# Optimization experiments

Hardware: AMD Instinct MI355X
Metric: run time of the kernel (lower is better)

The kernel has to match this reference:

```python
import jax, jax.numpy as jnp
import numpy as np

NUM_EXPERTS = 8
TOP_K = 2


def setup_inputs() -> dict:
    key = jax.random.key(0)
    k0, k1, k2, k3, k4 = jax.random.split(key, 5)
    T, D, F, E = 4096, 2048, 4096, NUM_EXPERTS  # tokens, hidden, intermediate, experts
    s_in = 1.0 / np.sqrt(D).astype(np.float32)
    s_mid = 1.0 / np.sqrt(F).astype(np.float32)
    return {
        "hidden_states": jax.random.normal(k0, (T, D), jnp.float32),
        "gate_w": jax.random.normal(k1, (D, E), jnp.float32) * s_in,   # router gate (no bias)
        "w1": jax.random.normal(k2, (E, D, F), jnp.float32) * s_in,     # expert gate proj
        "w3": jax.random.normal(k3, (E, D, F), jnp.float32) * s_in,     # expert up proj
        "w2": jax.random.normal(k4, (E, F, D), jnp.float32) * s_mid,    # expert down proj
    }


def reference(hidden_states, gate_w, w1, w3, w2):
    x = hidden_states  # [T, D] (original flattens any leading dims)
    # Router: logits in fp32 (router_logits.float()), softmax over ALL experts,
    # take top-k WITHOUT renormalization (renormalize=False).
    logits = (x @ gate_w).astype(jnp.float32)            # [T, E]
    probs = jax.nn.softmax(logits, axis=-1)              # [T, E]
    topk_w, topk_i = jax.lax.top_k(probs, TOP_K)         # [T, K]
    # Dense combine weights: zero for non-selected experts. [T, E]
    combine = jnp.sum(
        jax.nn.one_hot(topk_i, NUM_EXPERTS, dtype=x.dtype) * topk_w[..., None],
        axis=1,
    )

    # SwiGLU experts, vmapped over the expert axis (fixed, small E).
    def expert_fn(w1e, w3e, w2e):
        return (jax.nn.silu(x @ w1e) * (x @ w3e)) @ w2e  # [T, D]

    expert_out = jax.vmap(expert_fn)(w1, w3, w2)         # [E, T, D]
    return jnp.einsum("te,etd->td", combine, expert_out)  # [T, D]
```

## Files before the change

### kernel.cpp

```cpp
#include <hip/hip_runtime.h>
#include <hip/hip_bf16.h>

#define TK 4096
#define DD 2048
#define FF 4096
#define NE 8
#define BM 128
#define BN 128
#define BKR 32
#define BKG 64

typedef __attribute__((ext_vector_type(8))) short bf16x8;
typedef __attribute__((ext_vector_type(4))) short bf16x4;
typedef __attribute__((ext_vector_type(4))) float f32x4;

__device__ __forceinline__ unsigned short f2bf(float f) {
  return __builtin_bit_cast(unsigned short, __float2bfloat16(f));
}

__device__ __forceinline__ void gl16(const unsigned short* g, unsigned short* l) {
  __builtin_amdgcn_global_load_lds(
      (const __attribute__((address_space(1))) unsigned int*)g,
      (__attribute__((address_space(3))) unsigned int*)l, 16, 0, 0);
}

__device__ __forceinline__ int g_swz(int row) { return ((row >> 1) & 3) ^ ((row >> 3) & 3); }
__device__ __forceinline__ int swzoff(int row, int bir) {
  return row * 64 + ((((bir >> 4) ^ g_swz(row)) & 3) << 4) + (bir & 15);
}
__device__ __forceinline__ int permB(int f) {
  return (f & 0x60) | ((f & 3) << 3) | ((f >> 2) & 7);
}

__global__ void k_router(const float* __restrict__ x, const float* __restrict__ gw,
                         int* __restrict__ cnt, int* __restrict__ ltok,
                         float* __restrict__ lw, unsigned short* __restrict__ xb) {
  int tok = (blockIdx.x * blockDim.x + threadIdx.x) >> 6;
  int lane = threadIdx.x & 63;
  if (tok >= TK) return;
  const float* xr = x + (size_t)tok * DD;
  float a0=0,a1=0,a2=0,a3=0,a4=0,a5=0,a6=0,a7=0;
  for (int p = 0; p < DD / 256; ++p) {
    int d0 = p * 256 + lane * 4;
    f32x4 xv = *(const f32x4*)(xr + d0);
    if (xb) {
      bf16x4 t;
      t[0] = (short)f2bf(xv[0]); t[1] = (short)f2bf(xv[1]);
      t[2] = (short)f2bf(xv[2]); t[3] = (short)f2bf(xv[3]);
      *(bf16x4*)(xb + (size_t)tok * DD + d0) = t;
    }
#pragma unroll
    for (int j = 0; j < 4; ++j) {
      float xs = xv[j];
      const f32x4* g = (const f32x4*)(gw + (size_t)(d0 + j) * NE);
      f32x4 g0 = g[0], g1 = g[1];
      a0 += xs * g0[0]; a1 += xs * g0[1]; a2 += xs * g0[2]; a3 += xs * g0[3];
      a4 += xs * g1[0]; a5 += xs * g1[1]; a6 += xs * g1[2]; a7 += xs * g1[3];
    }
  }
#pragma unroll
  for (int s = 32; s > 0; s >>= 1) {
    a0 += __shfl_xor(a0, s, 64); a1 += __shfl_xor(a1, s, 64);
    a2 += __shfl_xor(a2, s, 64); a3 += __shfl_xor(a3, s, 64);
    a4 += __shfl_xor(a4, s, 64); a5 += __shfl_xor(a5, s, 64);
    a6 += __shfl_xor(a6, s, 64); a7 += __shfl_xor(a7, s, 64);
  }
  if (lane == 0) {
    float p_[NE] = {a0, a1, a2, a3, a4, a5, a6, a7};
    float m = p_[0];
#pragma unroll
    for (int e = 1; e < NE; ++e) m = fmaxf(m, p_[e]);
    float ssum = 0.f;
#pragma unroll
    for (int e = 0; e < NE; ++e) { p_[e] = __expf(p_[e] - m); ssum += p_[e]; }
    float inv = 1.f / ssum;
    int i1 = 0; float b1 = p_[0];
#pragma unroll
    for (int e = 1; e < NE; ++e) if (p_[e] > b1) { b1 = p_[e]; i1 = e; }
    int i2 = -1; float b2 = -1.f;
#pragma unroll
    for (int e = 0; e < NE; ++e) if (e != i1 && p_[e] > b2) { b2 = p_[e]; i2 = e; }
    int s1 = atomicAdd(&cnt[i1], 1);
    ltok[i1 * TK + s1] = tok; lw[i1 * TK + s1] = b1 * inv;
    int s2 = atomicAdd(&cnt[i2], 1);
    ltok[i2 * TK + s2] = tok; lw[i2 * TK + s2] = b2 * inv;
  }
}

__global__ void k_prefix(const int* __restrict__ cnt, int* __restrict__ off) {
  if (threadIdx.x == 0) {
    int a = 0;
#pragma unroll
    for (int e = 0; e < NE; ++e) { off[e] = a; a += cnt[e]; }
    off[NE] = a;
  }
}

__global__ void k_tr(const float* __restrict__ src0, unsigned short* __restrict__ dst0,
                     int R, int C) {
  const int e = blockIdx.z;
  const float* src = src0 + (size_t)e * R * C;
  unsigned short* dst = dst0 + (size_t)e * R * C;
  const int r0 = blockIdx.y * 64, c0 = blockIdx.x * 64;
  const int tid = threadIdx.x;
  __shared__ unsigned short t[64][66];
#pragma unroll
  for (int p = 0; p < 4; ++p) {
    int r = p * 16 + (tid >> 4);
    int c = (tid & 15) * 4;
    f32x4 v = *(const f32x4*)(src + (size_t)(r0 + r) * C + c0 + c);
#pragma unroll
    for (int j = 0; j < 4; ++j) t[c + j][r] = f2bf(v[j]);
  }
  __syncthreads();
#pragma unroll
  for (int p = 0; p < 2; ++p) {
    int c = p * 32 + (tid >> 3);
    int r = (tid & 7) * 8;
    bf16x8 o;
#pragma unroll
    for (int j = 0; j < 8; ++j) o[j] = (short)t[c][r + j];
    *(bf16x8*)(dst + (size_t)(c0 + c) * R + r0 + r) = o;
  }
}


__global__ __launch_bounds__(256, 2)
void k_gemm1g(const unsigned short* __restrict__ xb, const unsigned short* __restrict__ w1t,
              const unsigned short* __restrict__ w3t, const int* __restrict__ cnt,
              const int* __restrict__ off, const int* __restrict__ ltok,
              const float* __restrict__ lw, unsigned short* __restrict__ H) {
  const int e = blockIdx.z;
  const int ce = cnt[e];
  const int m0 = blockIdx.y * BM;
  if (m0 >= ce) return;
  const int n0 = blockIdx.x * BN;
  const int tid = threadIdx.x, lane = tid & 63, w = tid >> 6;
  const int wr = w >> 1, wc = w & 1;
  const unsigned short* W1 = w1t + (size_t)e * FF * DD;
  const unsigned short* W3 = w3t + (size_t)e * FF * DD;
  const int base = off[e];

  __shared__ __align__(16) unsigned short As[BM * BKG];
  __shared__ __align__(16) unsigned short B1s[BN * BKG];
  __shared__ __align__(16) unsigned short B3s[BN * BKG];

  const int swz8 = ((lane & 7) ^ ((lane >> 3) & 7)) * 8;
  const unsigned short* aSrc[4];
  const unsigned short* b1Src[4];
  const unsigned short* b3Src[4];
#pragma unroll
  for (int i = 0; i < 4; ++i) {
    int row = w * 32 + i * 8 + (lane >> 3);
    int gm = m0 + row;
    int tok = (gm < ce) ? ltok[e * TK + gm] : 0;
    aSrc[i]  = xb + (size_t)tok * DD + swz8;
    b1Src[i] = W1 + (size_t)(n0 + row) * DD + swz8;
    b3Src[i] = W3 + (size_t)(n0 + row) * DD + swz8;
  }

  int aOff[4][2], bOff[4][2];
#pragma unroll
  for (int m = 0; m < 4; ++m) {
    int row = wr * 64 + m * 16 + (lane & 15);
#pragma unroll
    for (int kk = 0; kk < 2; ++kk) {
      int c = kk * 4 + (lane >> 4);
      aOff[m][kk] = row * 128 + ((c ^ (row & 7)) << 4);
    }
  }
#pragma unroll
  for (int n = 0; n < 4; ++n) {
    int row = wc * 64 + n * 16 + (lane & 15);
#pragma unroll
    for (int kk = 0; kk < 2; ++kk) {
      int c = kk * 4 + (lane >> 4);
      bOff[n][kk] = row * 128 + ((c ^ (row & 7)) << 4);
    }
  }

  f32x4 acc1[4][4], acc3[4][4];
#pragma unroll
  for (int m = 0; m < 4; ++m)
#pragma unroll
    for (int n = 0; n < 4; ++n)
#pragma unroll
      for (int j = 0; j < 4; ++j) { acc1[m][n][j] = 0.f; acc3[m][n][j] = 0.f; }

  const int NT = DD / BKG;
  for (int kt = 0; kt < NT; ++kt) {
#pragma unroll
    for (int i = 0; i < 4; ++i) {
      const int seg = w * 4 + i;
      gl16(aSrc[i],  &As[seg * 512]);
      gl16(b1Src[i], &B1s[seg * 512]);
      gl16(b3Src[i], &B3s[seg * 512]);
      aSrc[i] += BKG; b1Src[i] += BKG; b3Src[i] += BKG;
    }
    __syncthreads();
#pragma unroll
    for (int kk = 0; kk < 2; ++kk) {
      bf16x8 af[4];
#pragma unroll
      for (int m = 0; m < 4; ++m) af[m] = *(const bf16x8*)((const char*)As + aOff[m][kk]);
#pragma unroll
      for (int n = 0; n < 4; ++n) {
        bf16x8 b1 = *(const bf16x8*)((const char*)B1s + bOff[n][kk]);
        bf16x8 b3 = *(const bf16x8*)((const char*)B3s + bOff[n][kk]);
#pragma unroll
        for (int m = 0; m < 4; ++m) {
          acc1[m][n] = __builtin_amdgcn_mfma_f32_16x16x32_bf16(af[m], b1, acc1[m][n], 0, 0, 0);
          acc3[m][n] = __builtin_amdgcn_mfma_f32_16x16x32_bf16(af[m], b3, acc3[m][n], 0, 0, 0);
        }
      }
    }
    __syncthreads();
  }

#pragma unroll
  for (int m = 0; m < 4; ++m) {
    const int rbase = wr * 64 + m * 16 + ((lane >> 4) << 2);
    float wts[4]; bool val[4];
#pragma unroll
    for (int j = 0; j < 4; ++j) {
      int r = m0 + rbase + j;
      val[j] = r < ce;
      wts[j] = val[j] ? lw[e * TK + r] : 0.f;
    }
#pragma unroll
    for (int n = 0; n < 4; ++n) {
      const int col = n0 + wc * 64 + n * 16 + (lane & 15);
#pragma unroll
      for (int j = 0; j < 4; ++j) {
        if (!val[j]) continue;
        float s1 = acc1[m][n][j], s3 = acc3[m][n][j];
        float h = s1 / (1.f + __expf(-s1)) * s3 * wts[j];
        H[(size_t)(base + m0 + rbase + j) * FF + col] = f2bf(h);
      }
    }
  }
}

__global__ __launch_bounds__(256, 3)
void k_gemm2g(const unsigned short* __restrict__ H, const unsigned short* __restrict__ w2t,
              const int* __restrict__ cnt, const int* __restrict__ off,
              const int* __restrict__ ltok, float* __restrict__ out) {
  const int e = blockIdx.z;
  const int ce = cnt[e];
  const int m0 = blockIdx.y * BM;
  if (m0 >= ce) return;
  const int n0 = blockIdx.x * BN;
  const int tid = threadIdx.x, lane = tid & 63, w = tid >> 6;
  const int wr = w >> 1, wc = w & 1;
  const unsigned short* W2 = w2t + (size_t)e * DD * FF;
  const int base = off[e];

  __shared__ __align__(16) unsigned short As[BM * BKG];
  __shared__ __align__(16) unsigned short Bs[BN * BKG];

  const int swz8 = ((lane & 7) ^ ((lane >> 3) & 7)) * 8;
  const unsigned short* aSrc[4];
  const unsigned short* bSrc[4];
#pragma unroll
  for (int i = 0; i < 4; ++i) {
    int row = w * 32 + i * 8 + (lane >> 3);
    int gm = m0 + row;
    int hr = (gm < ce) ? gm : 0;
    aSrc[i] = H + (size_t)(base + hr) * FF + swz8;
    bSrc[i] = W2 + (size_t)(n0 + row) * FF + swz8;
  }

  int aOff[4][2], bOff[4][2];
#pragma unroll
  for (int m = 0; m < 4; ++m) {
    int row = wr * 64 + m * 16 + (lane & 15);
#pragma unroll
    for (int kk = 0; kk < 2; ++kk) {
      int c = kk * 4 + (lane >> 4);
      aOff[m][kk] = row * 128 + ((c ^ (row & 7)) << 4);
    }
  }
#pragma unroll
  for (int n = 0; n < 4; ++n) {
    int row = wc * 64 + n * 16 + (lane & 15);
#pragma unroll
    for (int kk = 0; kk < 2; ++kk) {
      int c = kk * 4 + (lane >> 4);
      bOff[n][kk] = row * 128 + ((c ^ (row & 7)) << 4);
    }
  }

  f32x4 acc[4][4];
#pragma unroll
  for (int m = 0; m < 4; ++m)
#pragma unroll
    for (int n = 0; n < 4; ++n)
#pragma unroll
      for (int j = 0; j < 4; ++j) acc[m][n][j] = 0.f;

  const int NT = FF / BKG;
  for (int kt = 0; kt < NT; ++kt) {
#pragma unroll
    for (int i = 0; i < 4; ++i) {
      const int seg = w * 4 + i;
      gl16(aSrc[i], &As[seg * 512]);
      gl16(bSrc[i], &Bs[seg * 512]);
      aSrc[i] += BKG; bSrc[i] += BKG;
    }
    __syncthreads();
#pragma unroll
    for (int kk = 0; kk < 2; ++kk) {
      bf16x8 af[4];
#pragma unroll
      for (int m = 0; m < 4; ++m) af[m] = *(const bf16x8*)((const char*)As + aOff[m][kk]);
#pragma unroll
      for (int n = 0; n < 4; ++n) {
        bf16x8 bf = *(const bf16x8*)((const char*)Bs + bOff[n][kk]);
#pragma unroll
        for (int m = 0; m < 4; ++m)
          acc[m][n] = __builtin_amdgcn_mfma_f32_16x16x32_bf16(af[m], bf, acc[m][n], 0, 0, 0);
      }
    }
    __syncthreads();
  }

#pragma unroll
  for (int m = 0; m < 4; ++m) {
    const int rbase = wr * 64 + m * 16 + ((lane >> 4) << 2);
    int toks[4]; bool val[4];
#pragma unroll
    for (int j = 0; j < 4; ++j) {
      int r = m0 + rbase + j;
      val[j] = r < ce;
      toks[j] = val[j] ? ltok[e * TK + r] : 0;
    }
#pragma unroll
    for (int n = 0; n < 4; ++n) {
      const int col = n0 + wc * 64 + n * 16 + (lane & 15);
#pragma unroll
      for (int j = 0; j < 4; ++j)
        if (val[j]) atomicAdd(out + (size_t)toks[j] * DD + col, acc[m][n][j]);
    }
  }
}

__global__ __launch_bounds__(256, 2)
void k_gemm1(const float* __restrict__ x, const float* __restrict__ w1g,
             const float* __restrict__ w3g, const int* __restrict__ cnt,
             const int* __restrict__ off, const int* __restrict__ ltok,
             const float* __restrict__ lw, unsigned short* __restrict__ H) {
  const int e = blockIdx.z;
  const int ce = cnt[e];
  const int m0 = blockIdx.y * BM;
  if (m0 >= ce) return;
  const int n0 = blockIdx.x * BN;
  const int tid = threadIdx.x, lane = tid & 63, wv = tid >> 6;
  const int wr = wv >> 1, wc = wv & 1;
  const float* W1 = w1g + (size_t)e * DD * FF;
  const float* W3 = w3g + (size_t)e * DD * FF;
  const int base = off[e];

  __shared__ unsigned short As[2][BM * BKR];
  __shared__ unsigned short B1s[2][BN * BKR];
  __shared__ unsigned short B3s[2][BN * BKR];

  const int arow = tid >> 1, ah = tid & 1;
  const float* xrow = (m0 + arow < ce) ? (x + (size_t)ltok[e * TK + (m0 + arow)] * DD) : nullptr;
  const int dblk = tid >> 5, fblk = tid & 31;

  const int kb = (lane >> 4) * 16;
  int aOff[4], bOff[4], wAoff[4], wBoff[4];
#pragma unroll
  for (int m = 0; m < 4; ++m) aOff[m] = swzoff(wr * 64 + m * 16 + (lane & 15), kb);
#pragma unroll
  for (int n = 0; n < 4; ++n) bOff[n] = swzoff(permB(wc * 64 + n * 16 + (lane & 15)), kb);
#pragma unroll
  for (int j = 0; j < 4; ++j) {
    wAoff[j] = swzoff(arow, ah * 32 + j * 8);
    wBoff[j] = swzoff(permB(fblk * 4 + j), dblk * 8);
  }

  f32x4 acc1[4][4], acc3[4][4];
#pragma unroll
  for (int m = 0; m < 4; ++m)
#pragma unroll
    for (int n = 0; n < 4; ++n)
#pragma unroll
      for (int j = 0; j < 4; ++j) { acc1[m][n][j] = 0.f; acc3[m][n][j] = 0.f; }

  f32x4 av[4], v1[4], v3[4];

  auto LOAD = [&](int kt) {
    const int k0 = kt * BKR;
#pragma unroll
    for (int j = 0; j < 4; ++j) {
      if (xrow) av[j] = *(const f32x4*)(xrow + k0 + ah * 16 + j * 4);
      else { av[j][0] = 0.f; av[j][1] = 0.f; av[j][2] = 0.f; av[j][3] = 0.f; }
    }
    const float* p1 = W1 + (size_t)(k0 + dblk * 4) * FF + (n0 + fblk * 4);
    const float* p3 = W3 + (size_t)(k0 + dblk * 4) * FF + (n0 + fblk * 4);
#pragma unroll
    for (int r = 0; r < 4; ++r) {
      v1[r] = *(const f32x4*)(p1 + (size_t)r * FF);
      v3[r] = *(const f32x4*)(p3 + (size_t)r * FF);
    }
  };
  auto STORE = [&](int buf) {
#pragma unroll
    for (int j = 0; j < 4; ++j) {
      bf16x4 t;
      t[0] = (short)f2bf(av[j][0]); t[1] = (short)f2bf(av[j][1]);
      t[2] = (short)f2bf(av[j][2]); t[3] = (short)f2bf(av[j][3]);
      *(bf16x4*)((char*)As[buf] + wAoff[j]) = t;
    }
#pragma unroll
    for (int j = 0; j < 4; ++j) {
      bf16x4 t1, t3;
      t1[0] = (short)f2bf(v1[0][j]); t1[1] = (short)f2bf(v1[1][j]);
      t1[2] = (short)f2bf(v1[2][j]); t1[3] = (short)f2bf(v1[3][j]);
      t3[0] = (short)f2bf(v3[0][j]); t3[1] = (short)f2bf(v3[1][j]);
      t3[2] = (short)f2bf(v3[2][j]); t3[3] = (short)f2bf(v3[3][j]);
      *(bf16x4*)((char*)B1s[buf] + wBoff[j]) = t1;
      *(bf16x4*)((char*)B3s[buf] + wBoff[j]) = t3;
    }
  };

  LOAD(0); STORE(0);
  int cur = 0;
  const int NT = DD / BKR;
  for (int kt = 0; kt < NT; ++kt) {
    if (kt + 1 < NT) LOAD(kt + 1);
    __syncthreads();
    bf16x8 af[4];
#pragma unroll
    for (int m = 0; m < 4; ++m) af[m] = *(const bf16x8*)((const char*)As[cur] + aOff[m]);
#pragma unroll
    for (int n = 0; n < 4; ++n) {
      bf16x8 b1 = *(const bf16x8*)((const char*)B1s[cur] + bOff[n]);
      bf16x8 b3 = *(const bf16x8*)((const char*)B3s[cur] + bOff[n]);
#pragma unroll
      for (int m = 0; m < 4; ++m) {
        acc1[m][n] = __builtin_amdgcn_mfma_f32_16x16x32_bf16(af[m], b1, acc1[m][n], 0, 0, 0);
        acc3[m][n] = __builtin_amdgcn_mfma_f32_16x16x32_bf16(af[m], b3, acc3[m][n], 0, 0, 0);
      }
    }
    if (kt + 1 < NT) STORE(cur ^ 1);
    cur ^= 1;
  }

#pragma unroll
  for (int m = 0; m < 4; ++m) {
    const int rbase = wr * 64 + m * 16 + ((lane >> 4) << 2);
    float wts[4]; bool val[4];
#pragma unroll
    for (int j = 0; j < 4; ++j) {
      int r = m0 + rbase + j;
      val[j] = r < ce;
      wts[j] = val[j] ? lw[e * TK + r] : 0.f;
    }
#pragma unroll
    for (int n = 0; n < 4; ++n) {
      const int col = n0 + wc * 64 + n * 16 + (lane & 15);
#pragma unroll
      for (int j = 0; j < 4; ++j) {
        if (!val[j]) continue;
        float s1 = acc1[m][n][j], s3 = acc3[m][n][j];
        float h = s1 / (1.f + __expf(-s1)) * s3 * wts[j];
        H[(size_t)(base + m0 + rbase + j) * FF + col] = f2bf(h);
      }
    }
  }
}

__global__ __launch_bounds__(256, 2)
void k_gemm2(const unsigned short* __restrict__ H, const float* __restrict__ w2g,
             const int* __restrict__ cnt, const int* __restrict__ off,
             const int* __restrict__ ltok, float* __restrict__ out) {
  const int e = blockIdx.z;
  const int ce = cnt[e];
  const int m0 = blockIdx.y * BM;
  if (m0 >= ce) return;
  const int n0 = blockIdx.x * BN;
  const int tid = threadIdx.x, lane = tid & 63, wv = tid >> 6;
  const int wr = wv >> 1, wc = wv & 1;
  const float* W2 = w2g + (size_t)e * FF * DD;
  const int base = off[e];

  __shared__ unsigned short As[2][BM * BKR];
  __shared__ unsigned short Bs[2][BN * BKR];

  const int arow = tid >> 1, ah = tid & 1;
  const bool aval = (m0 + arow) < ce;
  const unsigned short* hrow = H + (size_t)(base + m0 + arow) * FF;
  const int kblk = tid >> 5, nblk = tid & 31;

  const int kb = (lane >> 4) * 16;
  int aOff[4], bOff[4], wAoff[2], wBoff[4];
#pragma unroll
  for (int m = 0; m < 4; ++m) aOff[m] = swzoff(wr * 64 + m * 16 + (lane & 15), kb);
#pragma unroll
  for (int n = 0; n < 4; ++n) bOff[n] = swzoff(permB(wc * 64 + n * 16 + (lane & 15)), kb);
#pragma unroll
  for (int j = 0; j < 2; ++j) wAoff[j] = swzoff(arow, ah * 32 + j * 16);
#pragma unroll
  for (int j = 0; j < 4; ++j) wBoff[j] = swzoff(permB(nblk * 4 + j), kblk * 8);

  f32x4 acc[4][4];
#pragma unroll
  for (int m = 0; m < 4; ++m)
#pragma unroll
    for (int n = 0; n < 4; ++n)
#pragma unroll
      for (int j = 0; j < 4; ++j) acc[m][n][j] = 0.f;

  bf16x8 av2[2];
  f32x4 wv2[4];

  auto LOAD = [&](int kt) {
    const int k0 = kt * BKR;
#pragma unroll
    for (int j = 0; j < 2; ++j) {
      if (aval) av2[j] = *(const bf16x8*)(hrow + k0 + ah * 16 + j * 8);
      else {
#pragma unroll
        for (int q = 0; q < 8; ++q) av2[j][q] = 0;
      }
    }
    const float* p = W2 + (size_t)(k0 + kblk * 4) * DD + (n0 + nblk * 4);
#pragma unroll
    for (int r = 0; r < 4; ++r) wv2[r] = *(const f32x4*)(p + (size_t)r * DD);
  };
  auto STORE = [&](int buf) {
#pragma unroll
    for (int j = 0; j < 2; ++j) *(bf16x8*)((char*)As[buf] + wAoff[j]) = av2[j];
#pragma unroll
    for (int j = 0; j < 4; ++j) {
      bf16x4 t;
      t[0] = (short)f2bf(wv2[0][j]); t[1] = (short)f2bf(wv2[1][j]);
      t[2] = (short)f2bf(wv2[2][j]); t[3] = (short)f2bf(wv2[3][j]);
      *(bf16x4*)((char*)Bs[buf] + wBoff[j]) = t;
    }
  };

  LOAD(0); STORE(0);
  int cur = 0;
  const int NT = FF / BKR;
  for (int kt = 0; kt < NT; ++kt) {
    if (kt + 1 < NT) LOAD(kt + 1);
    __syncthreads();
    bf16x8 af[4];
#pragma unroll
    for (int m = 0; m < 4; ++m) af[m] = *(const bf16x8*)((const char*)As[cur] + aOff[m]);
#pragma unroll
    for (int n = 0; n < 4; ++n) {
      bf16x8 bf = *(const bf16x8*)((const char*)Bs[cur] + bOff[n]);
#pragma unroll
      for (int m = 0; m < 4; ++m)
        acc[m][n] = __builtin_amdgcn_mfma_f32_16x16x32_bf16(af[m], bf, acc[m][n], 0, 0, 0);
    }
    if (kt + 1 < NT) STORE(cur ^ 1);
    cur ^= 1;
  }

#pragma unroll
  for (int m = 0; m < 4; ++m) {
    const int rbase = wr * 64 + m * 16 + ((lane >> 4) << 2);
    int toks[4]; bool val[4];
#pragma unroll
    for (int j = 0; j < 4; ++j) {
      int r = m0 + rbase + j;
      val[j] = r < ce;
      toks[j] = val[j] ? ltok[e * TK + r] : 0;
    }
#pragma unroll
    for (int n = 0; n < 4; ++n) {
      const int col = n0 + wc * 64 + n * 16 + (lane & 15);
#pragma unroll
      for (int j = 0; j < 4; ++j)
        if (val[j]) atomicAdd(out + (size_t)toks[j] * DD + col, acc[m][n][j]);
    }
  }
}

extern "C" void kernel_launch(void* const* d_in, const int* in_sizes, int n_in,
                              void* d_out, int out_size, void* d_ws, size_t ws_size,
                              hipStream_t stream) {
  const float* x  = (const float*)d_in[0];
  const float* gw = (const float*)d_in[1];
  const float* w1 = (const float*)d_in[2];
  const float* w3 = (const float*)d_in[3];
  const float* w2 = (const float*)d_in[4];
  float* out = (float*)d_out;

  char* ws = (char*)d_ws;
  int*   cnt  = (int*)(ws);
  int*   off  = (int*)(ws + 64);
  int*   ltok = (int*)(ws + 256);
  float* lw   = (float*)(ws + 256 + (size_t)NE * TK * 4);

  const size_t SZ_XB = (size_t)TK * DD * 2;
  const size_t SZ_W  = (size_t)NE * DD * FF * 2;
  const size_t SZ_H  = (size_t)2 * TK * FF * 2;
  size_t o = (size_t)1 << 20;
  unsigned short* xb  = (unsigned short*)(ws + o); o += SZ_XB;
  unsigned short* w1t = (unsigned short*)(ws + o); o += SZ_W;
  unsigned short* w3t = (unsigned short*)(ws + o); o += SZ_W;
  unsigned short* w2t = (unsigned short*)(ws + o); o += SZ_W;
  unsigned short* Hg  = (unsigned short*)(ws + o); o += SZ_H;
  const bool full = (ws_size >= o);

  hipMemsetAsync(cnt, 0, 64, stream);
  hipMemsetAsync(d_out, 0, (size_t)out_size * 4, stream);

  if (full) {
    k_router<<<dim3(TK / 4), 256, 0, stream>>>(x, gw, cnt, ltok, lw, xb);
    k_prefix<<<dim3(1), 64, 0, stream>>>(cnt, off);
    k_tr<<<dim3(FF / 64, DD / 64, NE), 256, 0, stream>>>(w1, w1t, DD, FF);
    k_tr<<<dim3(FF / 64, DD / 64, NE), 256, 0, stream>>>(w3, w3t, DD, FF);
    k_tr<<<dim3(DD / 64, FF / 64, NE), 256, 0, stream>>>(w2, w2t, FF, DD);
    k_gemm1g<<<dim3(FF / BN, TK / BM, NE), 256, 0, stream>>>(xb, w1t, w3t, cnt, off, ltok, lw, Hg);
    k_gemm2g<<<dim3(DD / BN, TK / BM, NE), 256, 0, stream>>>(Hg, w2t, cnt, off, ltok, out);
  } else {
    unsigned short* H = (unsigned short*)(ws + ((size_t)1 << 20));
    if (ws_size < ((size_t)1 << 20) + SZ_H) return;
    k_router<<<dim3(TK / 4), 256, 0, stream>>>(x, gw, cnt, ltok, lw, (unsigned short*)nullptr);
    k_prefix<<<dim3(1), 64, 0, stream>>>(cnt, off);
    k_gemm1<<<dim3(FF / BN, TK / BM, NE), 256, 0, stream>>>(x, w1, w3, cnt, off, ltok, lw, H);
    k_gemm2<<<dim3(DD / BN, TK / BM, NE), 256, 0, stream>>>(H, w2, cnt, off, ltok, out);
  }
}
```

Before: 962.9 us.

## Double-buffer LDS in grouped GEMMs and transpose weights via registers

```diff
diff --git a/kernel.cpp b/kernel.cpp
--- a/kernel.cpp
+++ b/kernel.cpp
@@ -8,7 +8,7 @@
 #define BM 128
 #define BN 128
 #define BKR 32
-#define BKG 64
+#define BKG 32
 
 typedef __attribute__((ext_vector_type(8))) short bf16x8;
 typedef __attribute__((ext_vector_type(4))) short bf16x4;
@@ -96,31 +96,25 @@
   }
 }
 
-__global__ void k_tr(const float* __restrict__ src0, unsigned short* __restrict__ dst0,
-                     int R, int C) {
+__global__ __launch_bounds__(256)
+void k_tr(const float* __restrict__ src0, unsigned short* __restrict__ dst0,
+          int R, int C) {
   const int e = blockIdx.z;
   const float* src = src0 + (size_t)e * R * C;
   unsigned short* dst = dst0 + (size_t)e * R * C;
-  const int r0 = blockIdx.y * 64, c0 = blockIdx.x * 64;
   const int tid = threadIdx.x;
-  __shared__ unsigned short t[64][66];
-#pragma unroll
-  for (int p = 0; p < 4; ++p) {
-    int r = p * 16 + (tid >> 4);
-    int c = (tid & 15) * 4;
-    f32x4 v = *(const f32x4*)(src + (size_t)(r0 + r) * C + c0 + c);
-#pragma unroll
-    for (int j = 0; j < 4; ++j) t[c + j][r] = f2bf(v[j]);
-  }
-  __syncthreads();
-#pragma unroll
-  for (int p = 0; p < 2; ++p) {
-    int c = p * 32 + (tid >> 3);
-    int r = (tid & 7) * 8;
+  const int w = tid >> 6, lane = tid & 63;
+  const int r0 = blockIdx.y * 256 + w * 64 + (lane >> 3) * 8;
+  const int c0 = blockIdx.x * 32 + (lane & 7) * 4;
+  f32x4 v[8];
+#pragma unroll
+  for (int j = 0; j < 8; ++j) v[j] = *(const f32x4*)(src + (size_t)(r0 + j) * C + c0);
+#pragma unroll
+  for (int jc = 0; jc < 4; ++jc) {
     bf16x8 o;
 #pragma unroll
-    for (int j = 0; j < 8; ++j) o[j] = (short)t[c][r + j];
-    *(bf16x8*)(dst + (size_t)(c0 + c) * R + r0 + r) = o;
+    for (int j = 0; j < 8; ++j) o[j] = (short)f2bf(v[j][jc]);
+    *(bf16x8*)(dst + (size_t)(c0 + jc) * R + r0) = o;
   }
 }
 
@@ -141,42 +135,34 @@
   const unsigned short* W3 = w3t + (size_t)e * FF * DD;
   const int base = off[e];
 
-  __shared__ __align__(16) unsigned short As[BM * BKG];
-  __shared__ __align__(16) unsigned short B1s[BN * BKG];
-  __shared__ __align__(16) unsigned short B3s[BN * BKG];
-
-  const int swz8 = ((lane & 7) ^ ((lane >> 3) & 7)) * 8;
-  const unsigned short* aSrc[4];
-  const unsigned short* b1Src[4];
-  const unsigned short* b3Src[4];
-#pragma unroll
-  for (int i = 0; i < 4; ++i) {
-    int row = w * 32 + i * 8 + (lane >> 3);
+  __shared__ __align__(16) unsigned short As[2][BM * BKG];
+  __shared__ __align__(16) unsigned short B1s[2][BN * BKG];
+  __shared__ __align__(16) unsigned short B3s[2][BN * BKG];
+
+  const int rr = lane >> 2;
+  const int csrc = ((lane & 3) ^ ((lane >> 3) & 3)) * 8;
+  const unsigned short *aSrc[2], *b1Src[2], *b3Src[2];
+#pragma unroll
+  for (int i = 0; i < 2; ++i) {
+    int row = (w * 2 + i) * 16 + rr;
     int gm = m0 + row;
-    int tok = (gm < ce) ? ltok[e * TK + gm] : 0;
-    aSrc[i]  = xb + (size_t)tok * DD + swz8;
-    b1Src[i] = W1 + (size_t)(n0 + row) * DD + swz8;
-    b3Src[i] = W3 + (size_t)(n0 + row) * DD + swz8;
-  }
-
-  int aOff[4][2], bOff[4][2];
+    int tok = (gm < ce) ? ltok[e * TK + gm] : ltok[e * TK];
+    aSrc[i]  = xb + (size_t)tok * DD + csrc;
+    b1Src[i] = W1 + (size_t)(n0 + row) * DD + csrc;
+    b3Src[i] = W3 + (size_t)(n0 + row) * DD + csrc;
+  }
+
+  const int kc = lane >> 4;
+  int aOff[4], bOff[4];
 #pragma unroll
   for (int m = 0; m < 4; ++m) {
     int row = wr * 64 + m * 16 + (lane & 15);
-#pragma unroll
-    for (int kk = 0; kk < 2; ++kk) {
-      int c = kk * 4 + (lane >> 4);
-      aOff[m][kk] = row * 128 + ((c ^ (row & 7)) << 4);
-    }
+    aOff[m] = row * 64 + ((kc ^ ((row >> 1) & 3)) << 4);
   }
 #pragma unroll
   for (int n = 0; n < 4; ++n) {
     int row = wc * 64 + n * 16 + (lane & 15);
-#pragma unroll
-    for (int kk = 0; kk < 2; ++kk) {
-      int c = kk * 4 + (lane >> 4);
-      bOff[n][kk] = row * 128 + ((c ^ (row & 7)) << 4);
-    }
+    bOff[n] = row * 64 + ((kc ^ ((row >> 1) & 3)) << 4);
   }
 
   f32x4 acc1[4][4], acc3[4][4];
@@ -187,34 +173,38 @@
 #pragma unroll
       for (int j = 0; j < 4; ++j) { acc1[m][n][j] = 0.f; acc3[m][n][j] = 0.f; }
 
+  auto STAGE = [&](int buf) {
+#pragma unroll
+    for (int i = 0; i < 2; ++i) {
+      const int seg = w * 2 + i;
+      gl16(aSrc[i],  &As[buf][seg * 512]);
+      gl16(b1Src[i], &B1s[buf][seg * 512]);
+      gl16(b3Src[i], &B3s[buf][seg * 512]);
+      aSrc[i] += BKG; b1Src[i] += BKG; b3Src[i] += BKG;
+    }
+  };
+
+  STAGE(0);
+  __syncthreads();
+  int cur = 0;
   const int NT = DD / BKG;
   for (int kt = 0; kt < NT; ++kt) {
-#pragma unroll
-    for (int i = 0; i < 4; ++i) {
-      const int seg = w * 4 + i;
-      gl16(aSrc[i],  &As[seg * 512]);
-      gl16(b1Src[i], &B1s[seg * 512]);
-      gl16(b3Src[i], &B3s[seg * 512]);
-      aSrc[i] += BKG; b1Src[i] += BKG; b3Src[i] += BKG;
+    if (kt + 1 < NT) STAGE(cur ^ 1);
+    bf16x8 af[4];
+#pragma unroll
+    for (int m = 0; m < 4; ++m) af[m] = *(const bf16x8*)((const char*)As[cur] + aOff[m]);
+#pragma unroll
+    for (int n = 0; n < 4; ++n) {
+      bf16x8 b1 = *(const bf16x8*)((const char*)B1s[cur] + bOff[n]);
+      bf16x8 b3 = *(const bf16x8*)((const char*)B3s[cur] + bOff[n]);
+#pragma unroll
+      for (int m = 0; m < 4; ++m) {
+        acc1[m][n] = __builtin_amdgcn_mfma_f32_16x16x32_bf16(af[m], b1, acc1[m][n], 0, 0, 0);
+        acc3[m][n] = __builtin_amdgcn_mfma_f32_16x16x32_bf16(af[m], b3, acc3[m][n], 0, 0, 0);
+      }
     }
     __syncthreads();
-#pragma unroll
-    for (int kk = 0; kk < 2; ++kk) {
-      bf16x8 af[4];
-#pragma unroll
-      for (int m = 0; m < 4; ++m) af[m] = *(const bf16x8*)((const char*)As + aOff[m][kk]);
-#pragma unroll
-      for (int n = 0; n < 4; ++n) {
-        bf16x8 b1 = *(const bf16x8*)((const char*)B1s + bOff[n][kk]);
-        bf16x8 b3 = *(const bf16x8*)((const char*)B3s + bOff[n][kk]);
-#pragma unroll
-        for (int m = 0; m < 4; ++m) {
-          acc1[m][n] = __builtin_amdgcn_mfma_f32_16x16x32_bf16(af[m], b1, acc1[m][n], 0, 0, 0);
-          acc3[m][n] = __builtin_amdgcn_mfma_f32_16x16x32_bf16(af[m], b3, acc3[m][n], 0, 0, 0);
-        }
-      }
-    }
-    __syncthreads();
+    cur ^= 1;
   }
 
 #pragma unroll
@@ -255,39 +245,32 @@
   const unsigned short* W2 = w2t + (size_t)e * DD * FF;
   const int base = off[e];
 
-  __shared__ __align__(16) unsigned short As[BM * BKG];
-  __shared__ __align__(16) unsigned short Bs[BN * BKG];
-
-  const int swz8 = ((lane & 7) ^ ((lane >> 3) & 7)) * 8;
-  const unsigned short* aSrc[4];
-  const unsigned short* bSrc[4];
-#pragma unroll
-  for (int i = 0; i < 4; ++i) {
-    int row = w * 32 + i * 8 + (lane >> 3);
+  __shared__ __align__(16) unsigned short As[2][BM * BKG];
+  __shared__ __align__(16) unsigned short Bs[2][BN * BKG];
+
+  const int rr = lane >> 2;
+  const int csrc = ((lane & 3) ^ ((lane >> 3) & 3)) * 8;
+  const unsigned short *aSrc[2], *bSrc[2];
+#pragma unroll
+  for (int i = 0; i < 2; ++i) {
+    int row = (w * 2 + i) * 16 + rr;
     int gm = m0 + row;
     int hr = (gm < ce) ? gm : 0;
-    aSrc[i] = H + (size_t)(base + hr) * FF + swz8;
-    bSrc[i] = W2 + (size_t)(n0 + row) * FF + swz8;
-  }
-
-  int aOff[4][2], bOff[4][2];
+    aSrc[i] = H + (size_t)(base + hr) * FF + csrc;
+    bSrc[i] = W2 + (size_t)(n0 + row) * FF + csrc;
+  }
+
+  const int kc = lane >> 4;
+  int aOff[4], bOff[4];
 #pragma unroll
   for (int m = 0; m < 4; ++m) {
     int row = wr * 64 + m * 16 + (lane & 15);
-#pragma unroll
-    for (int kk = 0; kk < 2; ++kk) {
-      int c = kk * 4 + (lane >> 4);
-      aOff[m][kk] = row * 128 + ((c ^ (row & 7)) << 4);
-    }
+    aOff[m] = row * 64 + ((kc ^ ((row >> 1) & 3)) << 4);
   }
 #pragma unroll
   for (int n = 0; n < 4; ++n) {
     int row = wc * 64 + n * 16 + (lane & 15);
-#pragma unroll
-    for (int kk = 0; kk < 2; ++kk) {
-      int c = kk * 4 + (lane >> 4);
-      bOff[n][kk] = row * 128 + ((c ^ (row & 7)) << 4);
-    }
+    bOff[n] = row * 64 + ((kc ^ ((row >> 1) & 3)) << 4);
   }
 
   f32x4 acc[4][4];
@@ -298,30 +281,34 @@
 #pragma unroll
       for (int j = 0; j < 4; ++j) acc[m][n][j] = 0.f;
 
+  auto STAGE = [&](int buf) {
+#pragma unroll
+    for (int i = 0; i < 2; ++i) {
+      const int seg = w * 2 + i;
+      gl16(aSrc[i], &As[buf][seg * 512]);
+      gl16(bSrc[i], &Bs[buf][seg * 512]);
+      aSrc[i] += BKG; bSrc[i] += BKG;
+    }
+  };
+
+  STAGE(0);
+  __syncthreads();
+  int cur = 0;
   const int NT = FF / BKG;
   for (int kt = 0; kt < NT; ++kt) {
-#pragma unroll
-    for (int i = 0; i < 4; ++i) {
-      const int seg = w * 4 + i;
-      gl16(aSrc[i], &As[seg * 512]);
-      gl16(bSrc[i], &Bs[seg * 512]);
-      aSrc[i] += BKG; bSrc[i] += BKG;
+    if (kt + 1 < NT) STAGE(cur ^ 1);
+    bf16x8 af[4];
+#pragma unroll
+    for (int m = 0; m < 4; ++m) af[m] = *(const bf16x8*)((const char*)As[cur] + aOff[m]);
+#pragma unroll
+    for (int n = 0; n < 4; ++n) {
+      bf16x8 bf = *(const bf16x8*)((const char*)Bs[cur] + bOff[n]);
+#pragma unroll
+      for (int m = 0; m < 4; ++m)
+        acc[m][n] = __builtin_amdgcn_mfma_f32_16x16x32_bf16(af[m], bf, acc[m][n], 0, 0, 0);
     }
     __syncthreads();
-#pragma unroll
-    for (int kk = 0; kk < 2; ++kk) {
-      bf16x8 af[4];
-#pragma unroll
-      for (int m = 0; m < 4; ++m) af[m] = *(const bf16x8*)((const char*)As + aOff[m][kk]);
-#pragma unroll
-      for (int n = 0; n < 4; ++n) {
-        bf16x8 bf = *(const bf16x8*)((const char*)Bs + bOff[n][kk]);
-#pragma unroll
-        for (int m = 0; m < 4; ++m)
-          acc[m][n] = __builtin_amdgcn_mfma_f32_16x16x32_bf16(af[m], bf, acc[m][n], 0, 0, 0);
-      }
-    }
-    __syncthreads();
+    cur ^= 1;
   }
 
 #pragma unroll
@@ -615,9 +602,9 @@
   if (full) {
     k_router<<<dim3(TK / 4), 256, 0, stream>>>(x, gw, cnt, ltok, lw, xb);
     k_prefix<<<dim3(1), 64, 0, stream>>>(cnt, off);
-    k_tr<<<dim3(FF / 64, DD / 64, NE), 256, 0, stream>>>(w1, w1t, DD, FF);
-    k_tr<<<dim3(FF / 64, DD / 64, NE), 256, 0, stream>>>(w3, w3t, DD, FF);
-    k_tr<<<dim3(DD / 64, FF / 64, NE), 256, 0, stream>>>(w2, w2t, FF, DD);
+    k_tr<<<dim3(FF / 32, DD / 256, NE), 256, 0, stream>>>(w1, w1t, DD, FF);
+    k_tr<<<dim3(FF / 32, DD / 256, NE), 256, 0, stream>>>(w3, w3t, DD, FF);
+    k_tr<<<dim3(DD / 32, FF / 256, NE), 256, 0, stream>>>(w2, w2t, FF, DD);
     k_gemm1g<<<dim3(FF / BN, TK / BM, NE), 256, 0, stream>>>(xb, w1t, w3t, cnt, off, ltok, lw, Hg);
     k_gemm2g<<<dim3(DD / BN, TK / BM, NE), 256, 0, stream>>>(Hg, w2t, cnt, off, ltok, out);
   } else {
```

New measurement: 1.155 ms. 20.0% more time.

## Double-buffer weight tiles in expert GEMMs and transpose weights via registers

Applied to the files above, without the earlier changes.

```diff
diff --git a/kernel.cpp b/kernel.cpp
--- a/kernel.cpp
+++ b/kernel.cpp
@@ -8,7 +8,7 @@
 #define BM 128
 #define BN 128
 #define BKR 32
-#define BKG 64
+#define BKP 64
 
 typedef __attribute__((ext_vector_type(8))) short bf16x8;
 typedef __attribute__((ext_vector_type(4))) short bf16x4;
@@ -23,6 +23,9 @@
       (const __attribute__((address_space(1))) unsigned int*)g,
       (__attribute__((address_space(3))) unsigned int*)l, 16, 0, 0);
 }
+
+#define VMCNT(n) asm volatile("s_waitcnt vmcnt(" #n ")" ::: "memory")
+#define SBAR()   __builtin_amdgcn_s_barrier()
 
 __device__ __forceinline__ int g_swz(int row) { return ((row >> 1) & 3) ^ ((row >> 3) & 3); }
 __device__ __forceinline__ int swzoff(int row, int bir) {
@@ -96,31 +99,25 @@
   }
 }
 
-__global__ void k_tr(const float* __restrict__ src0, unsigned short* __restrict__ dst0,
-                     int R, int C) {
+__global__ __launch_bounds__(256)
+void k_tr(const float* __restrict__ src0, unsigned short* __restrict__ dst0,
+          int R, int C) {
   const int e = blockIdx.z;
   const float* src = src0 + (size_t)e * R * C;
   unsigned short* dst = dst0 + (size_t)e * R * C;
-  const int r0 = blockIdx.y * 64, c0 = blockIdx.x * 64;
   const int tid = threadIdx.x;
-  __shared__ unsigned short t[64][66];
-#pragma unroll
-  for (int p = 0; p < 4; ++p) {
-    int r = p * 16 + (tid >> 4);
-    int c = (tid & 15) * 4;
-    f32x4 v = *(const f32x4*)(src + (size_t)(r0 + r) * C + c0 + c);
-#pragma unroll
-    for (int j = 0; j < 4; ++j) t[c + j][r] = f2bf(v[j]);
-  }
-  __syncthreads();
-#pragma unroll
-  for (int p = 0; p < 2; ++p) {
-    int c = p * 32 + (tid >> 3);
-    int r = (tid & 7) * 8;
+  const int w = tid >> 6, lane = tid & 63;
+  const int r0 = blockIdx.y * 256 + w * 64 + (lane >> 3) * 8;
+  const int c0 = blockIdx.x * 32 + (lane & 7) * 4;
+  f32x4 v[8];
+#pragma unroll
+  for (int j = 0; j < 8; ++j) v[j] = *(const f32x4*)(src + (size_t)(r0 + j) * C + c0);
+#pragma unroll
+  for (int jc = 0; jc < 4; ++jc) {
     bf16x8 o;
 #pragma unroll
-    for (int j = 0; j < 8; ++j) o[j] = (short)t[c][r + j];
-    *(bf16x8*)(dst + (size_t)(c0 + c) * R + r0 + r) = o;
+    for (int j = 0; j < 8; ++j) o[j] = (short)f2bf(v[j][jc]);
+    *(bf16x8*)(dst + (size_t)(c0 + jc) * R + r0) = o;
   }
 }
 
@@ -141,31 +138,30 @@
   const unsigned short* W3 = w3t + (size_t)e * FF * DD;
   const int base = off[e];
 
-  __shared__ __align__(16) unsigned short As[BM * BKG];
-  __shared__ __align__(16) unsigned short B1s[BN * BKG];
-  __shared__ __align__(16) unsigned short B3s[BN * BKG];
+  __shared__ __align__(16) unsigned short As[BM * BKP];
+  __shared__ __align__(16) unsigned short B1s[2][BM * BKP];
+  __shared__ __align__(16) unsigned short B3s[2][BM * BKP];
 
   const int swz8 = ((lane & 7) ^ ((lane >> 3) & 7)) * 8;
-  const unsigned short* aSrc[4];
-  const unsigned short* b1Src[4];
-  const unsigned short* b3Src[4];
+  const unsigned short *aSrc[4], *b1Src[4], *b3Src[4];
 #pragma unroll
   for (int i = 0; i < 4; ++i) {
     int row = w * 32 + i * 8 + (lane >> 3);
     int gm = m0 + row;
-    int tok = (gm < ce) ? ltok[e * TK + gm] : 0;
+    int tok = (gm < ce) ? ltok[e * TK + gm] : ltok[e * TK];
     aSrc[i]  = xb + (size_t)tok * DD + swz8;
     b1Src[i] = W1 + (size_t)(n0 + row) * DD + swz8;
     b3Src[i] = W3 + (size_t)(n0 + row) * DD + swz8;
   }
 
+  const int kc = lane >> 4;
   int aOff[4][2], bOff[4][2];
 #pragma unroll
   for (int m = 0; m < 4; ++m) {
     int row = wr * 64 + m * 16 + (lane & 15);
 #pragma unroll
     for (int kk = 0; kk < 2; ++kk) {
-      int c = kk * 4 + (lane >> 4);
+      int c = kk * 4 + kc;
       aOff[m][kk] = row * 128 + ((c ^ (row & 7)) << 4);
     }
   }
@@ -174,7 +170,7 @@
     int row = wc * 64 + n * 16 + (lane & 15);
 #pragma unroll
     for (int kk = 0; kk < 2; ++kk) {
-      int c = kk * 4 + (lane >> 4);
+      int c = kk * 4 + kc;
       bOff[n][kk] = row * 128 + ((c ^ (row & 7)) << 4);
     }
   }
@@ -187,17 +183,23 @@
 #pragma unroll
       for (int j = 0; j < 4; ++j) { acc1[m][n][j] = 0.f; acc3[m][n][j] = 0.f; }
 
-  const int NT = DD / BKG;
-  for (int kt = 0; kt < NT; ++kt) {
+  auto STAGE_A = [&]() {
+#pragma unroll
+    for (int i = 0; i < 4; ++i) {
+      gl16(aSrc[i], &As[(w * 4 + i) * 512]);
+      aSrc[i] += BKP;
+    }
+  };
+  auto STAGE_B = [&](int buf) {
 #pragma unroll
     for (int i = 0; i < 4; ++i) {
       const int seg = w * 4 + i;
-      gl16(aSrc[i],  &As[seg * 512]);
-      gl16(b1Src[i], &B1s[seg * 512]);
-      gl16(b3Src[i], &B3s[seg * 512]);
-      aSrc[i] += BKG; b1Src[i] += BKG; b3Src[i] += BKG;
-    }
-    __syncthreads();
+      gl16(b1Src[i], &B1s[buf][seg * 512]);
+      gl16(b3Src[i], &B3s[buf][seg * 512]);
+      b1Src[i] += BKP; b3Src[i] += BKP;
+    }
+  };
+  auto COMPUTE = [&](int buf) {
 #pragma unroll
     for (int kk = 0; kk < 2; ++kk) {
       bf16x8 af[4];
@@ -205,8 +207,8 @@
       for (int m = 0; m < 4; ++m) af[m] = *(const bf16x8*)((const char*)As + aOff[m][kk]);
 #pragma unroll
       for (int n = 0; n < 4; ++n) {
-        bf16x8 b1 = *(const bf16x8*)((const char*)B1s + bOff[n][kk]);
-        bf16x8 b3 = *(const bf16x8*)((const char*)B3s + bOff[n][kk]);
+        bf16x8 b1 = *(const bf16x8*)((const char*)B1s[buf] + bOff[n][kk]);
+        bf16x8 b3 = *(const bf16x8*)((const char*)B3s[buf] + bOff[n][kk]);
 #pragma unroll
         for (int m = 0; m < 4; ++m) {
           acc1[m][n] = __builtin_amdgcn_mfma_f32_16x16x32_bf16(af[m], b1, acc1[m][n], 0, 0, 0);
@@ -214,8 +216,24 @@
         }
       }
     }
-    __syncthreads();
-  }
+  };
+
+  const int NT = DD / BKP;
+  STAGE_A();
+  STAGE_B(0);
+  int b = 0;
+  for (int kt = 0; kt < NT - 1; ++kt) {
+    STAGE_B(b ^ 1);
+    VMCNT(8);
+    SBAR();
+    COMPUTE(b);
+    SBAR();
+    STAGE_A();
+    b ^= 1;
+  }
+  VMCNT(0);
+  SBAR();
+  COMPUTE(b);
 
 #pragma unroll
   for (int m = 0; m < 4; ++m) {
@@ -255,12 +273,11 @@
   const unsigned short* W2 = w2t + (size_t)e * DD * FF;
   const int base = off[e];
 
-  __shared__ __align__(16) unsigned short As[BM * BKG];
-  __shared__ __align__(16) unsigned short Bs[BN * BKG];
+  __shared__ __align__(16) unsigned short As[BM * BKP];
+  __shared__ __align__(16) unsigned short Bs[2][BM * BKP];
 
   const int swz8 = ((lane & 7) ^ ((lane >> 3) & 7)) * 8;
-  const unsigned short* aSrc[4];
-  const unsigned short* bSrc[4];
+  const unsigned short *aSrc[4], *bSrc[4];
 #pragma unroll
   for (int i = 0; i < 4; ++i) {
     int row = w * 32 + i * 8 + (lane >> 3);
@@ -270,13 +287,14 @@
     bSrc[i] = W2 + (size_t)(n0 + row) * FF + swz8;
   }
 
+  const int kc = lane >> 4;
   int aOff[4][2], bOff[4][2];
 #pragma unroll
   for (int m = 0; m < 4; ++m) {
     int row = wr * 64 + m * 16 + (lane & 15);
 #pragma unroll
     for (int kk = 0; kk < 2; ++kk) {
-      int c = kk * 4 + (lane >> 4);
+      int c = kk * 4 + kc;
       aOff[m][kk] = row * 128 + ((c ^ (row & 7)) << 4);
     }
   }
@@ -285,7 +303,7 @@
     int row = wc * 64 + n * 16 + (lane & 15);
 #pragma unroll
     for (int kk = 0; kk < 2; ++kk) {
-      int c = kk * 4 + (lane >> 4);
+      int c = kk * 4 + kc;
       bOff[n][kk] = row * 128 + ((c ^ (row & 7)) << 4);
     }
   }
@@ -298,16 +316,21 @@
 #pragma unroll
       for (int j = 0; j < 4; ++j) acc[m][n][j] = 0.f;
 
-  const int NT = FF / BKG;
-  for (int kt = 0; kt < NT; ++kt) {
+  auto STAGE_A = [&]() {
 #pragma unroll
     for (int i = 0; i < 4; ++i) {
-      const int seg = w * 4 + i;
-      gl16(aSrc[i], &As[seg * 512]);
-      gl16(bSrc[i], &Bs[seg * 512]);
-      aSrc[i] += BKG; bSrc[i] += BKG;
-    }
-    __syncthreads();
+      gl16(aSrc[i], &As[(w * 4 + i) * 512]);
+      aSrc[i] += BKP;
+    }
+  };
+  auto STAGE_B = [&](int buf) {
+#pragma unroll
+    for (int i = 0; i < 4; ++i) {
+      gl16(bSrc[i], &Bs[buf][(w * 4 + i) * 512]);
+      bSrc[i] += BKP;
+    }
+  };
+  auto COMPUTE = [&](int buf) {
 #pragma unroll
     for (int kk = 0; kk < 2; ++kk) {
       bf16x8 af[4];
@@ -315,14 +338,30 @@
       for (int m = 0; m < 4; ++m) af[m] = *(const bf16x8*)((const char*)As + aOff[m][kk]);
 #pragma unroll
       for (int n = 0; n < 4; ++n) {
-        bf16x8 bf = *(const bf16x8*)((const char*)Bs + bOff[n][kk]);
+        bf16x8 bf = *(const bf16x8*)((const char*)Bs[buf] + bOff[n][kk]);
 #pragma unroll
         for (int m = 0; m < 4; ++m)
           acc[m][n] = __builtin_amdgcn_mfma_f32_16x16x32_bf16(af[m], bf, acc[m][n], 0, 0, 0);
       }
     }
-    __syncthreads();
-  }
+  };
+
+  const int NT = FF / BKP;
+  STAGE_A();
+  STAGE_B(0);
+  int b = 0;
+  for (int kt = 0; kt < NT - 1; ++kt) {
+    STAGE_B(b ^ 1);
+    VMCNT(4);
+    SBAR();
+    COMPUTE(b);
+    SBAR();
+    STAGE_A();
+    b ^= 1;
+  }
+  VMCNT(0);
+  SBAR();
+  COMPUTE(b);
 
 #pragma unroll
   for (int m = 0; m < 4; ++m) {
@@ -615,9 +654,9 @@
   if (full) {
     k_router<<<dim3(TK / 4), 256, 0, stream>>>(x, gw, cnt, ltok, lw, xb);
     k_prefix<<<dim3(1), 64, 0, stream>>>(cnt, off);
-    k_tr<<<dim3(FF / 64, DD / 64, NE), 256, 0, stream>>>(w1, w1t, DD, FF);
-    k_tr<<<dim3(FF / 64, DD / 64, NE), 256, 0, stream>>>(w3, w3t, DD, FF);
-    k_tr<<<dim3(DD / 64, FF / 64, NE), 256, 0, stream>>>(w2, w2t, FF, DD);
+    k_tr<<<dim3(FF / 32, DD / 256, NE), 256, 0, stream>>>(w1, w1t, DD, FF);
+    k_tr<<<dim3(FF / 32, DD / 256, NE), 256, 0, stream>>>(w3, w3t, DD, FF);
+    k_tr<<<dim3(DD / 32, FF / 256, NE), 256, 0, stream>>>(w2, w2t, FF, DD);
     k_gemm1g<<<dim3(FF / BN, TK / BM, NE), 256, 0, stream>>>(xb, w1t, w3t, cnt, off, ltok, lw, Hg);
     k_gemm2g<<<dim3(DD / BN, TK / BM, NE), 256, 0, stream>>>(Hg, w2t, cnt, off, ltok, out);
   } else {
```

New measurement: 938.3 us. -2.6%, faster.
